# Kernel optimization log

Hardware: AMD Instinct MI355X
Metric: run time of the kernel (lower is better)

## Reference

```python
import jax, jax.numpy as jnp
import numpy as np
from jax import lax

NH, KD, AR, RES = 4, 16, 4, 40          # num_heads, key_dim, attn_ratio, resolution
DIM = 256
HD = DIM // NH                           # head_dim = 64
D = AR * KD                              # per-head value dim = 64
N = RES * RES                            # 1600 tokens
B = 16
EPS = 1e-5
SCALE = KD ** -0.5


def _bn(x, g, b, m, v):
    # eval-mode BatchNorm2d over channel dim of [B,C,H,W]
    s = g * lax.rsqrt(v + EPS)
    return (x - m[:, None, None]) * s[:, None, None] + b[:, None, None]


def setup_inputs() -> dict:
    key = jax.random.key(0)
    ks = iter(jax.random.split(key, 40))
    nrm = lambda sh, s=0.05: jax.random.normal(next(ks), sh, jnp.float32) * s
    pos = lambda sh: jax.random.uniform(next(ks), sh, jnp.float32, 0.5, 1.5)
    return {
        "x": jax.random.normal(next(ks), (B, DIM, RES, RES), jnp.float32),
        "dw_w": nrm((NH, HD, 1, 5, 5), 0.1),
        "dw_g": pos((NH, HD)), "dw_b": nrm((NH, HD)), "dw_m": nrm((NH, HD), 0.1), "dw_v": pos((NH, HD)),
        "q_w": nrm((NH, KD, HD), 0.1),
        "q_g": pos((NH, KD)), "q_b": nrm((NH, KD)), "q_m": nrm((NH, KD), 0.1), "q_v": pos((NH, KD)),
        "k_w": nrm((NH, KD, HD), 0.1),
        "k_g": pos((NH, KD)), "k_b": nrm((NH, KD)), "k_m": nrm((NH, KD), 0.1), "k_v": pos((NH, KD)),
        "v_w": nrm((NH, D, HD), 0.1),
        "v_g": pos((NH, D)), "v_b": nrm((NH, D)), "v_m": nrm((NH, D), 0.1), "v_v": pos((NH, D)),
        "proj_w": nrm((DIM, D * NH), 0.05),
        "proj_g": pos((DIM,)), "proj_b": nrm((DIM,)), "proj_m": nrm((DIM,), 0.1), "proj_v": pos((DIM,)),
        "attn_bias": nrm((NH, N), 0.02),
    }


def reference(x, dw_w, dw_g, dw_b, dw_m, dw_v,
              q_w, q_g, q_b, q_m, q_v,
              k_w, k_g, k_b, k_m, k_v,
              v_w, v_g, v_b, v_m, v_v,
              proj_w, proj_g, proj_b, proj_m, proj_v,
              attn_bias):
    Bx, C, H, W = x.shape
    Nx = H * W
    x_heads = jnp.split(x, NH, axis=1)   # NH x [B, HD, H, W]
    outs, prev = [], None
    for i in range(NH):
        # depthwise 5x5 conv + BN
        xi = lax.conv_general_dilated(
            x_heads[i], dw_w[i], window_strides=(1, 1), padding='SAME',
            feature_group_count=HD, dimension_numbers=('NCHW', 'OIHW', 'NCHW'))
        xi = _bn(xi, dw_g[i], dw_b[i], dw_m[i], dw_v[i])
        if prev is not None:
            xi = xi + prev                       # cascading residual
        # 1x1 conv projections + BN
        q = _bn(jnp.einsum('kc,bchw->bkhw', q_w[i], xi), q_g[i], q_b[i], q_m[i], q_v[i])
        k = _bn(jnp.einsum('kc,bchw->bkhw', k_w[i], xi), k_g[i], k_b[i], k_m[i], k_v[i])
        v = _bn(jnp.einsum('dc,bchw->bdhw', v_w[i], xi), v_g[i], v_b[i], v_m[i], v_v[i])
        qf = q.reshape(Bx, KD, Nx).transpose(0, 2, 1)   # [B, N, KD]
        kf = k.reshape(Bx, KD, Nx)                      # [B, KD, N]
        vf = v.reshape(Bx, D, Nx).transpose(0, 2, 1)    # [B, N, D]
        attn = jnp.einsum('bnk,bkm->bnm', qf, kf) * SCALE
        attn = attn + attn_bias[i][None, None, :]
        attn = jax.nn.softmax(attn, axis=-1)
        out = jnp.einsum('bnm,bmd->bnd', attn, vf).transpose(0, 2, 1).reshape(Bx, D, H, W)
        outs.append(out)
        prev = out[:, :HD]
    o = jnp.concatenate(outs, axis=1)                  # [B, D*NH, H, W]
    o = _bn(jnp.einsum('oc,bchw->bohw', proj_w, o), proj_g, proj_b, proj_m, proj_v)
    return jax.nn.relu(o)
```

## Files before the change

kernel.cpp:

```cpp
#include <hip/hip_runtime.h>
#include <cstddef>

namespace {
constexpr int kNH  = 4;
constexpr int kKD  = 16;
constexpr int kHD  = 64;
constexpr int kD   = 64;
constexpr int kRES = 40;
constexpr int kN   = 1600;
constexpr int kB   = 16;
constexpr int kDIM = 256;
constexpr int kQT  = kN / 32;
constexpr float kEPS   = 1e-5f;
constexpr float kSCALE = 0.25f;
constexpr float kLOG2E = 1.4426950408889634f;
constexpr float kC1    = kSCALE * kLOG2E;
}

typedef __attribute__((ext_vector_type(8)))  short short8;
typedef __attribute__((ext_vector_type(4)))  short s16x4;
typedef __attribute__((ext_vector_type(4)))  float f32x4;
typedef __attribute__((ext_vector_type(16))) float f32x16;

static __device__ __forceinline__ unsigned short f2bf(float x) {
  unsigned u = __builtin_bit_cast(unsigned, x);
  u = (u + 0x7fffu + ((u >> 16) & 1u)) >> 16;
  return (unsigned short)u;
}

struct Params {
  const float *x, *dw_w, *dw_g, *dw_b, *dw_m, *dw_v;
  const float *q_w, *q_g, *q_b, *q_m, *q_v;
  const float *k_w, *k_g, *k_b, *k_m, *k_v;
  const float *v_w, *v_g, *v_b, *v_m, *v_v;
  const float *proj_w, *proj_g, *proj_b, *proj_m, *proj_v, *attn_bias;
  float *cbn, *bias2, *psc, *psh, *qkv_sc, *qkv_sh;
  unsigned short *q_t, *k_t, *v_p, *o_bf, *w_bf, *x_t, *w_qk, *w_vv;
  float *out;
};


static __device__ __forceinline__ void prep_body(int i, const Params& p) {
  if (i < kNH * kN) p.bias2[i] = p.attn_bias[i] * kLOG2E;
  if (i < kDIM * kDIM) p.w_bf[i] = f2bf(p.proj_w[i]);
  if (i < kDIM) {
    const float sc = p.proj_g[i] * rsqrtf(p.proj_v[i] + kEPS);
    p.psc[i] = sc;
    p.psh[i] = p.proj_b[i] - p.proj_m[i] * sc;
  }
  if (i < kNH * 32 * kHD) {
    const int head = i >> 11;
    const int ch = (i >> 6) & 31;
    const int c = i & 63;
    const float wv = (ch < 16) ? p.q_w[head * 1024 + ch * 64 + c]
                               : p.k_w[head * 1024 + (ch - 16) * 64 + c];
    p.w_qk[i] = f2bf(wv);
  }
  if (i < kNH * kD * kHD) p.w_vv[i] = f2bf(p.v_w[i]);
  if (i < kNH * 96) {
    const int head = i / 96;
    const int ch = i - head * 96;
    float g, bb, mm, vv;
    if (ch < 16) {
      const int r = head * 16 + ch;
      g = p.q_g[r]; bb = p.q_b[r]; mm = p.q_m[r]; vv = p.q_v[r];
    } else if (ch < 32) {
      const int r = head * 16 + (ch - 16);
      g = p.k_g[r]; bb = p.k_b[r]; mm = p.k_m[r]; vv = p.k_v[r];
    } else {
      const int r = head * 64 + (ch - 32);
      g = p.v_g[r]; bb = p.v_b[r]; mm = p.v_m[r]; vv = p.v_v[r];
    }
    const float sc = g * rsqrtf(vv + kEPS);
    p.qkv_sc[i] = sc;
    p.qkv_sh[i] = bb - mm * sc;
  }
}

__global__ __launch_bounds__(256) void conv_prep_kernel(Params p) {
  const int blk = blockIdx.x;
  const int tid = threadIdx.x;
  if (blk < 256) prep_body(blk * 256 + tid, p);

  __shared__ float P[44 * 44];
  const int b = blk >> 8;
  const int gc = blk & 255;
  const int head = gc >> 6;
  const int c = gc & 63;

  for (int i = tid; i < 44 * 44; i += 256) P[i] = 0.f;
  __syncthreads();

  const float* xin = p.x + ((size_t)b * kDIM + gc) * kN;
  for (int i = tid; i < kN; i += 256) {
    const int r = i / kRES;
    const int col = i - r * kRES;
    P[(r + 2) * 44 + col + 2] = xin[i];
  }

  float wreg[25];
  const float* wc = p.dw_w + (size_t)gc * 25;
#pragma unroll
  for (int t = 0; t < 25; ++t) wreg[t] = wc[t];
  const float sc = p.dw_g[gc] * rsqrtf(p.dw_v[gc] + kEPS);
  const float sh = p.dw_b[gc] - p.dw_m[gc] * sc;

  __syncthreads();

  if (tid < 200) {
    const int h = tid / 5;
    const int w0 = (tid - h * 5) * 8;
    float acc[8] = {};
#pragma unroll
    for (int dh = 0; dh < 5; ++dh) {
      float t[12];
      const float* row = P + (h + dh) * 44 + w0;
#pragma unroll
      for (int i = 0; i < 12; ++i) t[i] = row[i];
#pragma unroll
      for (int j = 0; j < 8; ++j)
#pragma unroll
        for (int i = 0; i < 5; ++i)
          acc[j] = fmaf(t[j + i], wreg[dh * 5 + i], acc[j]);
    }
    float* xo = p.cbn + ((size_t)head * kB * kHD + (size_t)b * kHD + c) * kN +
                h * kRES + w0;
    f32x4 o0, o1;
#pragma unroll
    for (int j = 0; j < 4; ++j) {
      o0[j] = acc[j] * sc + sh;
      o1[j] = acc[4 + j] * sc + sh;
    }
    *(f32x4*)xo = o0;
    *(f32x4*)(xo + 4) = o1;
    if (head == 0) {
      unsigned short* xr = p.x_t + (((size_t)b * kN) + h * kRES + w0) * 64 + c;
#pragma unroll
      for (int j = 0; j < 4; ++j) {
        xr[(size_t)j * 64] = f2bf(o0[j]);
        xr[(size_t)(4 + j) * 64] = f2bf(o1[j]);
      }
    }
  }
}

__global__ __launch_bounds__(256) void qkv_mfma_kernel(Params p, int head) {
  const int lane = threadIdx.x & 63;
  const int w = blockIdx.x * 4 + (threadIdx.x >> 6);
  const unsigned short* x_t = p.x_t + (size_t)head * kB * kN * 64;
  const unsigned short* w_qk = p.w_qk + (size_t)head * 32 * kHD;
  const unsigned short* w_v = p.w_vv + (size_t)head * kD * kHD;
  const float* qsc = p.qkv_sc + head * 96;
  const float* qsh = p.qkv_sh + head * 96;

  const int b = w / 150;
  const int r = w - b * 150;
  const int col = lane & 31;
  const int h = lane >> 5;

  if (r < kQT) {
    const int n0 = r * 32;
    const unsigned short* ax = w_qk + (size_t)col * 64 + h * 8;
    const unsigned short* bx = x_t + ((size_t)b * kN + n0 + col) * 64 + h * 8;
    f32x16 acc = {};
#pragma unroll
    for (int kk = 0; kk < 4; ++kk) {
      const short8 af = *(const short8*)(ax + kk * 16);
      const short8 bf = *(const short8*)(bx + kk * 16);
      acc = __builtin_amdgcn_mfma_f32_32x32x16_bf16(af, bf, acc, 0, 0, 0);
    }
    const int n = n0 + col;
    unsigned short* qrow = p.q_t + ((size_t)b * kN + n) * 16;
    unsigned short* krow = p.k_t + ((size_t)b * kN + n) * 16;
#pragma unroll
    for (int g = 0; g < 4; ++g) {
      const int ch0 = g * 8 + 4 * h;
      const f32x4 s4 = *(const f32x4*)(qsc + ch0);
      const f32x4 h4 = *(const f32x4*)(qsh + ch0);
      s16x4 pk;
#pragma unroll
      for (int j = 0; j < 4; ++j)
        pk[j] = (short)f2bf(acc[g * 4 + j] * s4[j] + h4[j]);
      if (ch0 < 16) *(s16x4*)(qrow + ch0) = pk;
      else          *(s16x4*)(krow + ch0 - 16) = pk;
    }
  } else {
    const int idx = r - kQT;
    const int dt = idx / kQT;
    const int nt = idx - dt * kQT;
    const int n0 = nt * 32;
    const int d = dt * 32 + col;
    const unsigned short* ax = x_t + ((size_t)b * kN + n0 + col) * 64 + h * 8;
    const unsigned short* bx = w_v + (size_t)d * 64 + h * 8;
    f32x16 acc = {};
#pragma unroll
    for (int kk = 0; kk < 4; ++kk) {
      const short8 af = *(const short8*)(ax + kk * 16);
      const short8 bf = *(const short8*)(bx + kk * 16);
      acc = __builtin_amdgcn_mfma_f32_32x32x16_bf16(af, bf, acc, 0, 0, 0);
    }
    const float sc = qsc[32 + d];
    const float sh = qsh[32 + d];
    unsigned short* vrow = p.v_p + ((size_t)(b * kD) + d) * kN + n0;
#pragma unroll
    for (int g = 0; g < 4; ++g) {
      const int rr0 = g * 8 + 4 * h;
      const int low = rr0 & 15;
      const int pos = (rr0 & 16) | (low & 3) | ((low & 4) << 1) |
                      ((low & 8) >> 1);
      s16x4 pk;
#pragma unroll
      for (int j = 0; j < 4; ++j)
        pk[j] = (short)f2bf(acc[g * 4 + j] * sc + sh);
      *(s16x4*)(vrow + pos) = pk;
    }
  }
}

__global__ __launch_bounds__(256) void attn_fused_kernel(Params p, int head) {
  __shared__ float so[4][64][33];
  __shared__ float sml[4][32][2];
  const int tid = threadIdx.x;
  const int lane = tid & 63;
  const int wv = tid >> 6;
  const int blk = blockIdx.x;
  const int b = blk / kQT;
  const int qt = blk - b * kQT;
  const int col = lane & 31;
  const int h = lane >> 5;
  const int nq = qt * 32 + col;

  const short8 qf =
      *(const short8*)(p.q_t + ((size_t)b * kN + nq) * 16 + h * 8);
  const float* bs = p.bias2 + (size_t)head * kN;
  const unsigned short* vb0 = p.v_p + ((size_t)(b * kD) + col) * kN;
  const unsigned short* vb1 = p.v_p + ((size_t)(b * kD) + 32 + col) * kN;

  f32x16 o0 = {}, o1 = {};
  float m = -3.0e38f, l = 0.f;

  for (int kt = wv; kt < kQT; kt += 4) {
    const int kb = kt * 32;
    const short8 kf =
        *(const short8*)(p.k_t + ((size_t)b * kN + kb + col) * 16 + h * 8);
    f32x16 c = {};
    c = __builtin_amdgcn_mfma_f32_32x32x16_bf16(kf, qf, c, 0, 0, 0);

    const f32x4 bv0 = *(const f32x4*)(bs + kb + 4 * h);
    const f32x4 bv1 = *(const f32x4*)(bs + kb + 8 + 4 * h);
    const f32x4 bv2 = *(const f32x4*)(bs + kb + 16 + 4 * h);
    const f32x4 bv3 = *(const f32x4*)(bs + kb + 24 + 4 * h);

    float s[16];
#pragma unroll
    for (int r = 0; r < 4; ++r)  s[r]      = fmaf(c[r],      kC1, bv0[r]);
#pragma unroll
    for (int r = 0; r < 4; ++r)  s[4 + r]  = fmaf(c[4 + r],  kC1, bv1[r]);
#pragma unroll
    for (int r = 0; r < 4; ++r)  s[8 + r]  = fmaf(c[8 + r],  kC1, bv2[r]);
#pragma unroll
    for (int r = 0; r < 4; ++r)  s[12 + r] = fmaf(c[12 + r], kC1, bv3[r]);

    float tmax = s[0];
#pragma unroll
    for (int r = 1; r < 16; ++r) tmax = fmaxf(tmax, s[r]);
    tmax = fmaxf(tmax, __shfl_xor(tmax, 32));

    const bool upd = tmax > m + 8.0f;
    if (__any(upd)) {
      const float alpha = upd ? exp2f(m - tmax) : 1.0f;
      m = upd ? tmax : m;
      l *= alpha;
#pragma unroll
      for (int r = 0; r < 16; ++r) { o0[r] *= alpha; o1[r] *= alpha; }
    }

    short8 p0, p1;
    float lsum = 0.f;
#pragma unroll
    for (int e = 0; e < 8; ++e) {
      const float pe = exp2f(s[e] - m);
      lsum += pe;
      p0[e] = (short)f2bf(pe);
    }
#pragma unroll
    for (int e = 0; e < 8; ++e) {
      const float pe = exp2f(s[8 + e] - m);
      lsum += pe;
      p1[e] = (short)f2bf(pe);
    }
    l += lsum;

    const short8 vf00 = *(const short8*)(vb0 + kb + h * 8);
    const short8 vf01 = *(const short8*)(vb0 + kb + 16 + h * 8);
    const short8 vf10 = *(const short8*)(vb1 + kb + h * 8);
    const short8 vf11 = *(const short8*)(vb1 + kb + 16 + h * 8);
    o0 = __builtin_amdgcn_mfma_f32_32x32x16_bf16(vf00, p0, o0, 0, 0, 0);
    o0 = __builtin_amdgcn_mfma_f32_32x32x16_bf16(vf01, p1, o0, 0, 0, 0);
    o1 = __builtin_amdgcn_mfma_f32_32x32x16_bf16(vf10, p0, o1, 0, 0, 0);
    o1 = __builtin_amdgcn_mfma_f32_32x32x16_bf16(vf11, p1, o1, 0, 0, 0);
  }

  l += __shfl_xor(l, 32);

#pragma unroll
  for (int r = 0; r < 16; ++r) {
    so[wv][lane][r] = o0[r];
    so[wv][lane][16 + r] = o1[r];
  }
  if (h == 0) {
    sml[wv][col][0] = m;
    sml[wv][col][1] = l;
  }
  __syncthreads();

  float mc[4], lc[4];
  float M = -3.0e38f;
#pragma unroll
  for (int c = 0; c < 4; ++c) {
    mc[c] = sml[c][col][0];
    lc[c] = sml[c][col][1];
    M = fmaxf(M, mc[c]);
  }
  float scale[4];
  float lt = 0.f;
#pragma unroll
  for (int c = 0; c < 4; ++c) {
    scale[c] = exp2f(mc[c] - M);
    lt = fmaf(lc[c], scale[c], lt);
  }
  const float inv = 1.0f / lt;

  const int r0 = wv * 8;
  float ov[8];
#pragma unroll
  for (int j = 0; j < 8; ++j) {
    float a = 0.f;
#pragma unroll
    for (int c = 0; c < 4; ++c) a = fmaf(so[c][lane][r0 + j], scale[c], a);
    ov[j] = a * inv;
  }

  const int d0a = wv * 16 + 4 * h;
  const int d0b = d0a + 8;
  unsigned short* obf = p.o_bf + ((size_t)b * kN + nq) * kDIM + head * kD;
  s16x4 pa, pb;
  if (head < 3) {
    const float* cb = p.cbn + (size_t)(head + 1) * kB * kHD * kN +
                      (size_t)b * kHD * kN + nq;
    unsigned short* xrow = p.x_t + (size_t)(head + 1) * kB * kN * 64 +
                           ((size_t)b * kN + nq) * 64;
    s16x4 xa, xb;
#pragma unroll
    for (int j = 0; j < 4; ++j) {
      pa[j] = (short)f2bf(ov[j]);
      pb[j] = (short)f2bf(ov[4 + j]);
      xa[j] = (short)f2bf(cb[(size_t)(d0a + j) * kN] + ov[j]);
      xb[j] = (short)f2bf(cb[(size_t)(d0b + j) * kN] + ov[4 + j]);
    }
    *(s16x4*)(obf + d0a) = pa;
    *(s16x4*)(obf + d0b) = pb;
    *(s16x4*)(xrow + d0a) = xa;
    *(s16x4*)(xrow + d0b) = xb;
  } else {
#pragma unroll
    for (int j = 0; j < 4; ++j) {
      pa[j] = (short)f2bf(ov[j]);
      pb[j] = (short)f2bf(ov[4 + j]);
    }
    *(s16x4*)(obf + d0a) = pa;
    *(s16x4*)(obf + d0b) = pb;
  }
}

__global__ __launch_bounds__(256) void proj_mfma_kernel(Params p) {
  const int lane = threadIdx.x & 63;
  const int t = blockIdx.x * 4 + (threadIdx.x >> 6);
  const int b = t / 400;
  const int rem = t - b * 400;
  const int ot = rem / 50;
  const int nt = rem - ot * 50;
  const int col = lane & 31;
  const int h = lane >> 5;

  const unsigned short* arow =
      p.w_bf + ((size_t)(ot * 32 + col)) * kDIM + h * 8;
  const unsigned short* brow =
      p.o_bf + ((size_t)(b * kN + nt * 32 + col)) * kDIM + h * 8;

  f32x16 acc = {};
#pragma unroll
  for (int k = 0; k < 16; ++k) {
    const short8 af = *(const short8*)(arow + k * 16);
    const short8 bfr = *(const short8*)(brow + k * 16);
    acc = __builtin_amdgcn_mfma_f32_32x32x16_bf16(af, bfr, acc, 0, 0, 0);
  }

  float* ob = p.out + (size_t)b * kDIM * kN + nt * 32 + col;
#pragma unroll
  for (int r = 0; r < 16; ++r) {
    const int o = ot * 32 + (r & 3) + 8 * (r >> 2) + 4 * h;
    const float v = acc[r] * p.psc[o] + p.psh[o];
    ob[(size_t)o * kN] = fmaxf(v, 0.f);
  }
}

extern "C" void kernel_launch(void* const* d_in, const int* in_sizes, int n_in,
                              void* d_out, int out_size, void* d_ws,
                              size_t ws_size, hipStream_t stream) {
  Params p;
  p.x      = (const float*)d_in[0];
  p.dw_w   = (const float*)d_in[1];
  p.dw_g   = (const float*)d_in[2];
  p.dw_b   = (const float*)d_in[3];
  p.dw_m   = (const float*)d_in[4];
  p.dw_v   = (const float*)d_in[5];
  p.q_w    = (const float*)d_in[6];
  p.q_g    = (const float*)d_in[7];
  p.q_b    = (const float*)d_in[8];
  p.q_m    = (const float*)d_in[9];
  p.q_v    = (const float*)d_in[10];
  p.k_w    = (const float*)d_in[11];
  p.k_g    = (const float*)d_in[12];
  p.k_b    = (const float*)d_in[13];
  p.k_m    = (const float*)d_in[14];
  p.k_v    = (const float*)d_in[15];
  p.v_w    = (const float*)d_in[16];
  p.v_g    = (const float*)d_in[17];
  p.v_b    = (const float*)d_in[18];
  p.v_m    = (const float*)d_in[19];
  p.v_v    = (const float*)d_in[20];
  p.proj_w = (const float*)d_in[21];
  p.proj_g = (const float*)d_in[22];
  p.proj_b = (const float*)d_in[23];
  p.proj_m = (const float*)d_in[24];
  p.proj_v = (const float*)d_in[25];
  p.attn_bias = (const float*)d_in[26];

  float* ws = (float*)d_ws;
  p.cbn    = ws;
  p.bias2  = p.cbn + (size_t)kNH * kB * kHD * kN;
  p.psc    = p.bias2 + kNH * kN;
  p.psh    = p.psc + kDIM;
  p.qkv_sc = p.psh + kDIM;
  p.qkv_sh = p.qkv_sc + kNH * 96;
  p.q_t  = (unsigned short*)(p.qkv_sh + kNH * 96);
  p.k_t  = p.q_t + (size_t)kB * kN * kKD;
  p.v_p  = p.k_t + (size_t)kB * kN * kKD;
  p.o_bf = p.v_p + (size_t)kB * kD * kN;
  p.w_bf = p.o_bf + (size_t)kB * kN * kDIM;
  p.x_t  = p.w_bf + (size_t)kDIM * kDIM;
  p.w_qk = p.x_t + (size_t)kNH * kB * kN * 64;
  p.w_vv = p.w_qk + (size_t)kNH * 32 * kHD;
  p.out = (float*)d_out;

  conv_prep_kernel<<<kB * kDIM, 256, 0, stream>>>(p);

  for (int head = 0; head < kNH; ++head) {
    qkv_mfma_kernel<<<600, 256, 0, stream>>>(p, head);
    attn_fused_kernel<<<kB * kQT, 256, 0, stream>>>(p, head);
  }

  proj_mfma_kernel<<<1600, 256, 0, stream>>>(p);
}
```

Baseline: 352.0 us.

## Use linearity to precompute all-head QKV, fold residual update and projection into attention

The cascade residual is split by linearity. QKV for all heads is computed up front from the conv outputs in one launch. Each attention kernel then adds W·o_prev·scale into the next head's q/k/v buffers with an in-kernel MFMA. The last head's attention kernel also does the output projection, so the fp32 conv intermediate buffer and the separate projection and per-head QKV launches are gone. The cost is extra rounding from read-modify-write of bf16 q/k/v, and the projection now runs inside only 800 blocks.

```diff
diff --git a/kernel.cpp b/kernel.cpp
--- a/kernel.cpp
+++ b/kernel.cpp
@@ -27,6 +27,9 @@
   u = (u + 0x7fffu + ((u >> 16) & 1u)) >> 16;
   return (unsigned short)u;
 }
+static __device__ __forceinline__ float bf2f(unsigned short b) {
+  return __builtin_bit_cast(float, (unsigned)b << 16);
+}
 
 struct Params {
   const float *x, *dw_w, *dw_g, *dw_b, *dw_m, *dw_v;
@@ -34,11 +37,10 @@
   const float *k_w, *k_g, *k_b, *k_m, *k_v;
   const float *v_w, *v_g, *v_b, *v_m, *v_v;
   const float *proj_w, *proj_g, *proj_b, *proj_m, *proj_v, *attn_bias;
-  float *cbn, *bias2, *psc, *psh, *qkv_sc, *qkv_sh;
+  float *bias2, *psc, *psh, *qkv_sc, *qkv_sh;
   unsigned short *q_t, *k_t, *v_p, *o_bf, *w_bf, *x_t, *w_qk, *w_vv;
   float *out;
 };
-
 
 static __device__ __forceinline__ void prep_body(int i, const Params& p) {
   if (i < kNH * kN) p.bias2[i] = p.attn_bias[i] * kLOG2E;
@@ -123,35 +125,26 @@
         for (int i = 0; i < 5; ++i)
           acc[j] = fmaf(t[j + i], wreg[dh * 5 + i], acc[j]);
     }
-    float* xo = p.cbn + ((size_t)head * kB * kHD + (size_t)b * kHD + c) * kN +
-                h * kRES + w0;
-    f32x4 o0, o1;
-#pragma unroll
-    for (int j = 0; j < 4; ++j) {
-      o0[j] = acc[j] * sc + sh;
-      o1[j] = acc[4 + j] * sc + sh;
-    }
-    *(f32x4*)xo = o0;
-    *(f32x4*)(xo + 4) = o1;
-    if (head == 0) {
-      unsigned short* xr = p.x_t + (((size_t)b * kN) + h * kRES + w0) * 64 + c;
-#pragma unroll
-      for (int j = 0; j < 4; ++j) {
-        xr[(size_t)j * 64] = f2bf(o0[j]);
-        xr[(size_t)(4 + j) * 64] = f2bf(o1[j]);
-      }
-    }
-  }
-}
-
-__global__ __launch_bounds__(256) void qkv_mfma_kernel(Params p, int head) {
+    unsigned short* xr = p.x_t + (size_t)head * kB * kN * 64 +
+                         (((size_t)b * kN) + h * kRES + w0) * 64 + c;
+#pragma unroll
+    for (int j = 0; j < 8; ++j)
+      xr[(size_t)j * 64] = f2bf(acc[j] * sc + sh);
+  }
+}
+
+__global__ __launch_bounds__(256) void qkv_all_kernel(Params p) {
   const int lane = threadIdx.x & 63;
-  const int w = blockIdx.x * 4 + (threadIdx.x >> 6);
+  const int head = blockIdx.x / 600;
+  const int w = (blockIdx.x - head * 600) * 4 + (threadIdx.x >> 6);
   const unsigned short* x_t = p.x_t + (size_t)head * kB * kN * 64;
   const unsigned short* w_qk = p.w_qk + (size_t)head * 32 * kHD;
   const unsigned short* w_v = p.w_vv + (size_t)head * kD * kHD;
   const float* qsc = p.qkv_sc + head * 96;
   const float* qsh = p.qkv_sh + head * 96;
+  unsigned short* q_t = p.q_t + (size_t)head * kB * kN * kKD;
+  unsigned short* k_t = p.k_t + (size_t)head * kB * kN * kKD;
+  unsigned short* v_p = p.v_p + (size_t)head * kB * kD * kN;
 
   const int b = w / 150;
   const int r = w - b * 150;
@@ -170,8 +163,8 @@
       acc = __builtin_amdgcn_mfma_f32_32x32x16_bf16(af, bf, acc, 0, 0, 0);
     }
     const int n = n0 + col;
-    unsigned short* qrow = p.q_t + ((size_t)b * kN + n) * 16;
-    unsigned short* krow = p.k_t + ((size_t)b * kN + n) * 16;
+    unsigned short* qrow = q_t + ((size_t)b * kN + n) * 16;
+    unsigned short* krow = k_t + ((size_t)b * kN + n) * 16;
 #pragma unroll
     for (int g = 0; g < 4; ++g) {
       const int ch0 = g * 8 + 4 * h;
@@ -201,7 +194,7 @@
     }
     const float sc = qsc[32 + d];
     const float sh = qsh[32 + d];
-    unsigned short* vrow = p.v_p + ((size_t)(b * kD) + d) * kN + n0;
+    unsigned short* vrow = v_p + ((size_t)(b * kD) + d) * kN + n0;
 #pragma unroll
     for (int g = 0; g < 4; ++g) {
       const int rr0 = g * 8 + 4 * h;
@@ -220,6 +213,7 @@
 __global__ __launch_bounds__(256) void attn_fused_kernel(Params p, int head) {
   __shared__ float so[4][64][33];
   __shared__ float sml[4][32][2];
+  __shared__ unsigned short o_lds[32][72];
   const int tid = threadIdx.x;
   const int lane = tid & 63;
   const int wv = tid >> 6;
@@ -230,11 +224,15 @@
   const int h = lane >> 5;
   const int nq = qt * 32 + col;
 
+  const unsigned short* q_t = p.q_t + (size_t)head * kB * kN * kKD;
+  const unsigned short* k_t = p.k_t + (size_t)head * kB * kN * kKD;
+  const unsigned short* v_p = p.v_p + (size_t)head * kB * kD * kN;
+
   const short8 qf =
-      *(const short8*)(p.q_t + ((size_t)b * kN + nq) * 16 + h * 8);
+      *(const short8*)(q_t + ((size_t)b * kN + nq) * 16 + h * 8);
   const float* bs = p.bias2 + (size_t)head * kN;
-  const unsigned short* vb0 = p.v_p + ((size_t)(b * kD) + col) * kN;
-  const unsigned short* vb1 = p.v_p + ((size_t)(b * kD) + 32 + col) * kN;
+  const unsigned short* vb0 = v_p + ((size_t)(b * kD) + col) * kN;
+  const unsigned short* vb1 = v_p + ((size_t)(b * kD) + 32 + col) * kN;
 
   f32x16 o0 = {}, o1 = {};
   float m = -3.0e38f, l = 0.f;
@@ -242,7 +240,7 @@
   for (int kt = wv; kt < kQT; kt += 4) {
     const int kb = kt * 32;
     const short8 kf =
-        *(const short8*)(p.k_t + ((size_t)b * kN + kb + col) * 16 + h * 8);
+        *(const short8*)(k_t + ((size_t)b * kN + kb + col) * 16 + h * 8);
     f32x16 c = {};
     c = __builtin_amdgcn_mfma_f32_32x32x16_bf16(kf, qf, c, 0, 0, 0);
 
@@ -343,65 +341,96 @@
 
   const int d0a = wv * 16 + 4 * h;
   const int d0b = d0a + 8;
-  unsigned short* obf = p.o_bf + ((size_t)b * kN + nq) * kDIM + head * kD;
-  s16x4 pa, pb;
+#pragma unroll
+  for (int j = 0; j < 4; ++j) {
+    o_lds[col][d0a + j] = f2bf(ov[j]);
+    o_lds[col][d0b + j] = f2bf(ov[4 + j]);
+  }
   if (head < 3) {
-    const float* cb = p.cbn + (size_t)(head + 1) * kB * kHD * kN +
-                      (size_t)b * kHD * kN + nq;
-    unsigned short* xrow = p.x_t + (size_t)(head + 1) * kB * kN * 64 +
-                           ((size_t)b * kN + nq) * 64;
-    s16x4 xa, xb;
+    unsigned short* obf = p.o_bf + ((size_t)b * kN + nq) * kDIM + head * kD;
+    s16x4 pa, pb;
 #pragma unroll
     for (int j = 0; j < 4; ++j) {
       pa[j] = (short)f2bf(ov[j]);
       pb[j] = (short)f2bf(ov[4 + j]);
-      xa[j] = (short)f2bf(cb[(size_t)(d0a + j) * kN] + ov[j]);
-      xb[j] = (short)f2bf(cb[(size_t)(d0b + j) * kN] + ov[4 + j]);
     }
     *(s16x4*)(obf + d0a) = pa;
     *(s16x4*)(obf + d0b) = pb;
-    *(s16x4*)(xrow + d0a) = xa;
-    *(s16x4*)(xrow + d0b) = xb;
+  }
+  __syncthreads();
+
+  if (head < 3) {
+    const float* scn = p.qkv_sc + (head + 1) * 96;
+    if (wv == 0) {
+      const unsigned short* aw = p.w_qk + (size_t)(head + 1) * 32 * kHD +
+                                 (size_t)col * 64 + h * 8;
+      f32x16 acc = {};
+#pragma unroll
+      for (int kk = 0; kk < 4; ++kk) {
+        const short8 af = *(const short8*)(aw + kk * 16);
+        const short8 bf = *(const short8*)(&o_lds[col][kk * 16 + h * 8]);
+        acc = __builtin_amdgcn_mfma_f32_32x32x16_bf16(af, bf, acc, 0, 0, 0);
+      }
+      unsigned short* qrow = p.q_t + (size_t)(head + 1) * kB * kN * kKD +
+                             ((size_t)b * kN + nq) * 16;
+      unsigned short* krow = p.k_t + (size_t)(head + 1) * kB * kN * kKD +
+                             ((size_t)b * kN + nq) * 16;
+#pragma unroll
+      for (int r = 0; r < 16; ++r) {
+        const int ch = (r & 3) + 8 * (r >> 2) + 4 * h;
+        unsigned short* tp = (ch < 16) ? (qrow + ch) : (krow + ch - 16);
+        *tp = f2bf(bf2f(*tp) + acc[r] * scn[ch]);
+      }
+    } else if (wv <= 2) {
+      const int dbase = (wv - 1) * 32;
+      const unsigned short* aw = p.w_vv + (size_t)(head + 1) * kD * kHD +
+                                 (size_t)(dbase + col) * 64 + h * 8;
+      f32x16 acc = {};
+#pragma unroll
+      for (int kk = 0; kk < 4; ++kk) {
+        const short8 af = *(const short8*)(aw + kk * 16);
+        const short8 bf = *(const short8*)(&o_lds[col][kk * 16 + h * 8]);
+        acc = __builtin_amdgcn_mfma_f32_32x32x16_bf16(af, bf, acc, 0, 0, 0);
+      }
+      const int ml_ = nq & 15;
+      const int pos =
+          (nq & ~15) | (ml_ & 3) | ((ml_ & 4) << 1) | ((ml_ & 8) >> 1);
+      unsigned short* vbase = p.v_p + (size_t)(head + 1) * kB * kD * kN;
+#pragma unroll
+      for (int r = 0; r < 16; ++r) {
+        const int d = dbase + (r & 3) + 8 * (r >> 2) + 4 * h;
+        unsigned short* tp = vbase + ((size_t)(b * kD) + d) * kN + pos;
+        *tp = f2bf(bf2f(*tp) + acc[r] * scn[32 + d]);
+      }
+    }
   } else {
-#pragma unroll
-    for (int j = 0; j < 4; ++j) {
-      pa[j] = (short)f2bf(ov[j]);
-      pb[j] = (short)f2bf(ov[4 + j]);
-    }
-    *(s16x4*)(obf + d0a) = pa;
-    *(s16x4*)(obf + d0b) = pb;
-  }
-}
-
-__global__ __launch_bounds__(256) void proj_mfma_kernel(Params p) {
-  const int lane = threadIdx.x & 63;
-  const int t = blockIdx.x * 4 + (threadIdx.x >> 6);
-  const int b = t / 400;
-  const int rem = t - b * 400;
-  const int ot = rem / 50;
-  const int nt = rem - ot * 50;
-  const int col = lane & 31;
-  const int h = lane >> 5;
-
-  const unsigned short* arow =
-      p.w_bf + ((size_t)(ot * 32 + col)) * kDIM + h * 8;
-  const unsigned short* brow =
-      p.o_bf + ((size_t)(b * kN + nt * 32 + col)) * kDIM + h * 8;
-
-  f32x16 acc = {};
-#pragma unroll
-  for (int k = 0; k < 16; ++k) {
-    const short8 af = *(const short8*)(arow + k * 16);
-    const short8 bfr = *(const short8*)(brow + k * 16);
-    acc = __builtin_amdgcn_mfma_f32_32x32x16_bf16(af, bfr, acc, 0, 0, 0);
-  }
-
-  float* ob = p.out + (size_t)b * kDIM * kN + nt * 32 + col;
-#pragma unroll
-  for (int r = 0; r < 16; ++r) {
-    const int o = ot * 32 + (r & 3) + 8 * (r >> 2) + 4 * h;
-    const float v = acc[r] * p.psc[o] + p.psh[o];
-    ob[(size_t)o * kN] = fmaxf(v, 0.f);
+    const unsigned short* brow = p.o_bf + ((size_t)b * kN + nq) * kDIM;
+#pragma unroll
+    for (int gi = 0; gi < 2; ++gi) {
+      const int g = wv * 2 + gi;
+      const unsigned short* arow =
+          p.w_bf + (size_t)(g * 32 + col) * kDIM + h * 8;
+      f32x16 acc = {};
+#pragma unroll
+      for (int kk = 0; kk < 12; ++kk) {
+        const short8 af = *(const short8*)(arow + kk * 16);
+        const short8 bf = *(const short8*)(brow + kk * 16 + h * 8);
+        acc = __builtin_amdgcn_mfma_f32_32x32x16_bf16(af, bf, acc, 0, 0, 0);
+      }
+#pragma unroll
+      for (int kk = 12; kk < 16; ++kk) {
+        const short8 af = *(const short8*)(arow + kk * 16);
+        const short8 bf =
+            *(const short8*)(&o_lds[col][(kk - 12) * 16 + h * 8]);
+        acc = __builtin_amdgcn_mfma_f32_32x32x16_bf16(af, bf, acc, 0, 0, 0);
+      }
+#pragma unroll
+      for (int r = 0; r < 16; ++r) {
+        const int o = g * 32 + (r & 3) + 8 * (r >> 2) + 4 * h;
+        const float v = acc[r] * p.psc[o] + p.psh[o];
+        p.out[((size_t)b * kDIM + o) * kN + nq] = fmaxf(v, 0.f);
+      }
+    }
   }
 }
 
@@ -438,16 +467,15 @@
   p.attn_bias = (const float*)d_in[26];
 
   float* ws = (float*)d_ws;
-  p.cbn    = ws;
-  p.bias2  = p.cbn + (size_t)kNH * kB * kHD * kN;
+  p.bias2  = ws;
   p.psc    = p.bias2 + kNH * kN;
   p.psh    = p.psc + kDIM;
   p.qkv_sc = p.psh + kDIM;
   p.qkv_sh = p.qkv_sc + kNH * 96;
   p.q_t  = (unsigned short*)(p.qkv_sh + kNH * 96);
-  p.k_t  = p.q_t + (size_t)kB * kN * kKD;
-  p.v_p  = p.k_t + (size_t)kB * kN * kKD;
-  p.o_bf = p.v_p + (size_t)kB * kD * kN;
+  p.k_t  = p.q_t + (size_t)kNH * kB * kN * kKD;
+  p.v_p  = p.k_t + (size_t)kNH * kB * kN * kKD;
+  p.o_bf = p.v_p + (size_t)kNH * kB * kD * kN;
   p.w_bf = p.o_bf + (size_t)kB * kN * kDIM;
   p.x_t  = p.w_bf + (size_t)kDIM * kDIM;
   p.w_qk = p.x_t + (size_t)kNH * kB * kN * 64;
@@ -455,11 +483,7 @@
   p.out = (float*)d_out;
 
   conv_prep_kernel<<<kB * kDIM, 256, 0, stream>>>(p);
-
-  for (int head = 0; head < kNH; ++head) {
-    qkv_mfma_kernel<<<600, 256, 0, stream>>>(p, head);
+  qkv_all_kernel<<<kNH * 600, 256, 0, stream>>>(p);
+  for (int head = 0; head < kNH; ++head)
     attn_fused_kernel<<<kB * kQT, 256, 0, stream>>>(p, head);
-  }
-
-  proj_mfma_kernel<<<1600, 256, 0, stream>>>(p);
-}
+}
```

New measurement: 367.0 us. 1.04x slower.
